# Optimization experiments

Hardware: AMD Instinct MI355X
Metric: run time of the kernel (lower is better)

## Reference

```python
import jax, jax.numpy as jnp
import numpy as np

D, U, NNZ, B = 8192, 4096, 1_700_000, 1024

def setup_inputs() -> dict:
    key = jax.random.key(0)
    k1, k2, k3, k4 = jax.random.split(key, 4)
    x = jax.random.normal(k1, (B, D), dtype=jnp.float32)
    kernel_vector = jax.random.normal(k2, (NNZ,), dtype=jnp.float32) * 0.02
    bias = jax.random.normal(k3, (U,), dtype=jnp.float32) * 0.01
    flat = jax.random.randint(k4, (NNZ,), 0, D * U)  # random sparsity pattern
    nonzero_ind = jnp.stack([flat // U, flat % U], axis=1).astype(jnp.int32)  # [NNZ, 2]
    return {"x": x, "kernel_vector": kernel_vector, "bias": bias, "nonzero_ind": nonzero_ind}

def reference(x, kernel_vector, bias, nonzero_ind):
    # scatter_nd: build dense (D, U) kernel from nonzero entries (duplicates add, as in tf.scatter_nd)
    W = jnp.zeros((D, U), dtype=kernel_vector.dtype).at[nonzero_ind[:, 0], nonzero_ind[:, 1]].add(kernel_vector)
    out = x @ W + bias  # [B, U]
    return jnp.tanh(out)
```

## Files before the change

### kernel.cpp

```cpp
#include <hip/hip_runtime.h>
#include <hip/hip_fp16.h>
#include <cmath>

#define DIM_M 1024
#define DIM_K 8192
#define DIM_N 4096
#define SPLIT 4
#define KSPL  (DIM_K / SPLIT)
#define BKT   64
#define NT    (KSPL / BKT)
#define NB    1024
#define EPB   8192

typedef __attribute__((ext_vector_type(8))) _Float16 half8;
typedef __attribute__((ext_vector_type(4))) float floatx4;

struct __align__(8) Half4 { __half2 a, b; };

__device__ inline void gload_lds16(const void* g, void* l) {
    __builtin_amdgcn_global_load_lds(
        (const __attribute__((address_space(1))) void*)g,
        (__attribute__((address_space(3))) void*)l, 16, 0, 0);
}

__global__ void cvt_f2h(const floatx4* __restrict__ in, Half4* __restrict__ out, int n4) {
    int i = blockIdx.x * blockDim.x + threadIdx.x;
    if (i < n4) {
        floatx4 f = in[i];
        Half4 h;
        h.a = __floats2half2_rn(f.x, f.y);
        h.b = __floats2half2_rn(f.z, f.w);
        out[i] = h;
    }
}

__global__ __launch_bounds__(512) void cluster_k(const int* __restrict__ ind,
                                                 const float* __restrict__ kv,
                                                 uint2* __restrict__ ebuf,
                                                 unsigned* __restrict__ ofs,
                                                 int nnz) {
    extern __shared__ char csm[];
    uint2*    buf = (uint2*)csm;
    unsigned* cur = (unsigned*)(csm + 65536);
    unsigned* ss  = (unsigned*)(csm + 69632);
    const int tid = threadIdx.x, blk = blockIdx.x;
    const int base = blk * EPB;
    const int lim = min(nnz - base, EPB);
    const int4*   ip = (const int4*)(ind + 2 * (size_t)base);
    const float2* vp = (const float2*)(kv + base);

    for (int i = tid; i < NB; i += 512) cur[i] = 0u;
    __syncthreads();
    for (int k2 = tid; k2 < lim / 2; k2 += 512) {
        int4 w = ip[k2];
        atomicAdd(&cur[w.y >> 2], 1u);
        atomicAdd(&cur[w.w >> 2], 1u);
    }
    if ((lim & 1) && tid == 0) {
        int u = ind[2 * (size_t)(base + lim - 1) + 1];
        atomicAdd(&cur[u >> 2], 1u);
    }
    __syncthreads();
    unsigned c0 = cur[2 * tid], c1 = cur[2 * tid + 1];
    unsigned own = c0 + c1;
    ss[tid] = own;
    __syncthreads();
    for (int off = 1; off < 512; off <<= 1) {
        unsigned t = (tid >= off) ? ss[tid - off] : 0u;
        __syncthreads();
        ss[tid] += t;
        __syncthreads();
    }
    unsigned e0 = ss[tid] - own;
    unsigned e1 = e0 + c0;
    __syncthreads();
    cur[2 * tid]     = e0;
    cur[2 * tid + 1] = e1;
    unsigned* obase = ofs + (size_t)blk * (NB + 1);
    obase[2 * tid]     = e0;
    obase[2 * tid + 1] = e1;
    if (tid == 511) obase[NB] = ss[511];
    __syncthreads();
    for (int k2 = tid; k2 < lim / 2; k2 += 512) {
        int4 w = ip[k2];
        float2 v = vp[k2];
        unsigned r0 = atomicAdd(&cur[w.y >> 2], 1u);
        buf[r0] = make_uint2(((unsigned)(w.y & 3) << 13) | (unsigned)w.x, __float_as_uint(v.x));
        unsigned r1 = atomicAdd(&cur[w.w >> 2], 1u);
        buf[r1] = make_uint2(((unsigned)(w.w & 3) << 13) | (unsigned)w.z, __float_as_uint(v.y));
    }
    if ((lim & 1) && tid == 0) {
        size_t e = (size_t)base + lim - 1;
        int d = ind[2 * e], u = ind[2 * e + 1];
        unsigned r = atomicAdd(&cur[u >> 2], 1u);
        buf[r] = make_uint2(((unsigned)(u & 3) << 13) | (unsigned)d, __float_as_uint(kv[e]));
    }
    __syncthreads();
    for (int j = tid; j < lim; j += 512)
        ebuf[(size_t)blk * EPB + j] = buf[j];
}

__global__ __launch_bounds__(512) void accum_k(const uint2* __restrict__ ebuf,
                                               const unsigned* __restrict__ ofs,
                                               int nblk,
                                               Half4* __restrict__ wh4) {
    extern __shared__ float reg[];
    floatx4* reg4 = (floatx4*)reg;
    const int tid = threadIdx.x, bin = blockIdx.x;
    for (int i = tid; i < 8192; i += 512) reg4[i] = floatx4{0.f, 0.f, 0.f, 0.f};
    __syncthreads();
    for (int sb = tid; sb < nblk; sb += 512) {
        const unsigned* ob = ofs + (size_t)sb * (NB + 1) + bin;
        unsigned o0 = ob[0], o1 = ob[1];
        const uint2* p = ebuf + (size_t)sb * EPB;
        for (unsigned e = o0; e < o1; ++e) {
            uint2 v = p[e];
            atomicAdd(&reg[v.x], __uint_as_float(v.y));
        }
    }
    __syncthreads();
    for (int i = tid; i < 8192; i += 512) {
        floatx4 f = reg4[i];
        Half4 h;
        h.a = __floats2half2_rn(f.x, f.y);
        h.b = __floats2half2_rn(f.z, f.w);
        wh4[(size_t)bin * 8192 + i] = h;
    }
}

__global__ __launch_bounds__(1024, 4) void gemm8_k(
    const _Float16* __restrict__ Ah,
    const _Float16* __restrict__ Bh,
    _Float16*       __restrict__ part)
{
    extern __shared__ char smem[];

    const int tid  = threadIdx.x;
    const int lane = tid & 63;
    const int wave = tid >> 6;

    const int bid = blockIdx.x;
    const int swz = (bid & 7) * 32 + (bid >> 3);
    const int n0  = (swz >> 4) * 256;
    const int rem = swz & 15;
    const int m0  = (rem >> 2) * 256;
    const int sp  = rem & 3;
    const size_t kbase = (size_t)sp * KSPL;

    const int srow = tid >> 3;
    const int sch  = (tid & 7) ^ (srow & 7);
    const _Float16* aSg = Ah + (size_t)(m0 + srow) * DIM_K + kbase + sch * 8;
    const _Float16* bSg = Bh + (size_t)(n0 + srow) * DIM_K + kbase + sch * 8;
    char* aLg = smem + wave * 1024;
    char* bLg = smem + 32768 + wave * 1024;

    const int wn  = wave & 3;
    const int wrm = wave >> 2;
    const int q   = lane >> 4;
    const int l7  = lane & 7;
    const char* aRd = smem + (wrm * 64 + (lane & 15)) * 128;
    const char* bRd = smem + 32768 + (wn * 64 + (lane & 15)) * 128;
    const int ch0 = ((0 * 4 + q) ^ l7) * 16;
    const int ch1 = ((1 * 4 + q) ^ l7) * 16;

    floatx4 acc[4][4] = {};
    half8 aF[4], bF[4];

#define STAGE(C)                                                              \
    { _Pragma("unroll") for (int p = 0; p < 2; ++p) {                         \
        gload_lds16(aSg + (size_t)p * (128 * DIM_K), aLg + (C) * 65536 + p * 16384); \
        gload_lds16(bSg + (size_t)p * (128 * DIM_K), bLg + (C) * 65536 + p * 16384); } \
      aSg += BKT; bSg += BKT; }

#define PH(C, CH)                                                             \
    { _Pragma("unroll") for (int i = 0; i < 4; ++i)                           \
        aF[i] = *(const half8*)(aRd + (C) * 65536 + i * 2048 + (CH));         \
      _Pragma("unroll") for (int i = 0; i < 4; ++i)                           \
        bF[i] = *(const half8*)(bRd + (C) * 65536 + i * 2048 + (CH));         \
      asm volatile("s_waitcnt lgkmcnt(0)" ::: "memory");                      \
      __builtin_amdgcn_sched_barrier(0);                                      \
      __builtin_amdgcn_s_setprio(1);                                          \
      _Pragma("unroll") for (int mi = 0; mi < 4; ++mi)                        \
        _Pragma("unroll") for (int ni = 0; ni < 4; ++ni)                      \
          acc[mi][ni] = __builtin_amdgcn_mfma_f32_16x16x32_f16(               \
              aF[mi], bF[ni], acc[mi][ni], 0, 0, 0);                          \
      __builtin_amdgcn_s_setprio(0); }

#define KTILE(C) PH(C, ch0) PH(C, ch1)

    STAGE(0)
    STAGE(1)
    asm volatile("s_waitcnt vmcnt(4)" ::: "memory");
    __builtin_amdgcn_s_barrier();

    for (int t2 = 0; t2 < NT / 2; ++t2) {
        KTILE(0)
        __builtin_amdgcn_s_barrier();
        if (t2 < NT / 2 - 1) {
            STAGE(0)
            asm volatile("s_waitcnt vmcnt(4)" ::: "memory");
        } else {
            asm volatile("s_waitcnt vmcnt(0)" ::: "memory");
        }
        __builtin_amdgcn_s_barrier();
        KTILE(1)
        if (t2 < NT / 2 - 1) {
            __builtin_amdgcn_s_barrier();
            STAGE(1)
            asm volatile("s_waitcnt vmcnt(4)" ::: "memory");
            __builtin_amdgcn_s_barrier();
        }
    }

#undef KTILE
#undef PH
#undef STAGE

    _Float16* pbase = part + (size_t)sp * DIM_M * DIM_N;
    #pragma unroll
    for (int ni = 0; ni < 4; ++ni) {
        const int col = n0 + wn * 64 + ni * 16 + (lane & 15);
        #pragma unroll
        for (int mi = 0; mi < 4; ++mi) {
            const int row = m0 + wrm * 64 + mi * 16 + (q << 2);
            #pragma unroll
            for (int r = 0; r < 4; ++r)
                pbase[(size_t)(row + r) * DIM_N + col] = (_Float16)acc[mi][ni][r];
        }
    }
}

__global__ void reduce_tanh(const Half4* __restrict__ part, const float* __restrict__ bias,
                            floatx4* __restrict__ out) {
    const int n4 = DIM_M * DIM_N / 4;
    int i = blockIdx.x * blockDim.x + threadIdx.x;
    if (i < n4) {
        float sx = 0.f, sy = 0.f, sz = 0.f, sw = 0.f;
        #pragma unroll
        for (int sp = 0; sp < SPLIT; ++sp) {
            Half4 p = part[(size_t)sp * n4 + i];
            float2 lo = __half22float2(p.a);
            float2 hi = __half22float2(p.b);
            sx += lo.x; sy += lo.y; sz += hi.x; sw += hi.y;
        }
        floatx4 b = ((const floatx4*)bias)[i & (DIM_N / 4 - 1)];
        floatx4 o;
        o.x = tanhf(sx + b.x);
        o.y = tanhf(sy + b.y);
        o.z = tanhf(sz + b.z);
        o.w = tanhf(sw + b.w);
        out[i] = o;
    }
}

extern "C" void kernel_launch(void* const* d_in, const int* in_sizes, int n_in,
                              void* d_out, int out_size, void* d_ws, size_t ws_size,
                              hipStream_t stream) {
    const float* x    = (const float*)d_in[0];
    const float* kv   = (const float*)d_in[1];
    const float* bias = (const float*)d_in[2];
    const int*   ind  = (const int*)d_in[3];
    float* out = (float*)d_out;
    const int nnz = in_sizes[1];

    char* ws = (char*)d_ws;
    _Float16* wh = (_Float16*)ws;
    const size_t whBytes = (size_t)DIM_N * DIM_K * 2;
    _Float16* xh = (_Float16*)(ws + whBytes);
    const size_t xhBytes = (size_t)DIM_M * DIM_K * 2;
    _Float16* part = (_Float16*)(ws + whBytes + xhBytes);
    const size_t partBytes = (size_t)SPLIT * DIM_M * DIM_N * 2;
    uint2* ebuf = (uint2*)(ws + whBytes + xhBytes + partBytes);
    const size_t ebufBytes = (size_t)16 << 20;
    unsigned* ofs = (unsigned*)(ws + whBytes + xhBytes + partBytes + ebufBytes);

    const int xN4 = (int)((size_t)DIM_M * DIM_K / 4);
    const int oN4 = DIM_M * DIM_N / 4;
    const int nblk = (nnz + EPB - 1) / EPB;

    cvt_f2h<<<(xN4 + 255) / 256, 256, 0, stream>>>((const floatx4*)x, (Half4*)xh, xN4);

    hipFuncSetAttribute((const void*)cluster_k,
                        hipFuncAttributeMaxDynamicSharedMemorySize, 71680);
    cluster_k<<<nblk, 512, 71680, stream>>>(ind, kv, ebuf, ofs, nnz);

    hipFuncSetAttribute((const void*)accum_k,
                        hipFuncAttributeMaxDynamicSharedMemorySize, 131072);
    accum_k<<<NB, 512, 131072, stream>>>(ebuf, ofs, nblk, (Half4*)wh);

    hipFuncSetAttribute((const void*)gemm8_k,
                        hipFuncAttributeMaxDynamicSharedMemorySize, 131072);
    gemm8_k<<<dim3(256), 1024, 131072, stream>>>(xh, wh, part);

    reduce_tanh<<<(oN4 + 255) / 256, 256, 0, stream>>>((const Half4*)part, bias, (floatx4*)out);
}
```

Baseline: 125.2 us.

## Fuse x fp16 conversion into cluster kernel and split accum work per bin

The separate fp32-to-fp16 conversion kernel for x is folded into cluster_k as extra blocks appended after the clustering blocks, so both jobs run in one launch and can overlap. Separately, accum_k now gives each source block's bin segment to two threads that take alternating entries, doubling the parallelism in the scatter-accumulate loop. The conversion blocks still request 70KB of LDS they do not use, which can limit how many blocks fit per CU. The accum change adds more LDS atomic contention.

```diff
diff --git a/kernel.cpp b/kernel.cpp
--- a/kernel.cpp
+++ b/kernel.cpp
@@ -11,6 +11,7 @@
 #define NT    (KSPL / BKT)
 #define NB    1024
 #define EPB   8192
+#define CVTB  1024
 
 typedef __attribute__((ext_vector_type(8))) _Float16 half8;
 typedef __attribute__((ext_vector_type(4))) float floatx4;
@@ -23,27 +24,35 @@
         (__attribute__((address_space(3))) void*)l, 16, 0, 0);
 }
 
-__global__ void cvt_f2h(const floatx4* __restrict__ in, Half4* __restrict__ out, int n4) {
-    int i = blockIdx.x * blockDim.x + threadIdx.x;
-    if (i < n4) {
-        floatx4 f = in[i];
-        Half4 h;
-        h.a = __floats2half2_rn(f.x, f.y);
-        h.b = __floats2half2_rn(f.z, f.w);
-        out[i] = h;
-    }
-}
-
 __global__ __launch_bounds__(512) void cluster_k(const int* __restrict__ ind,
                                                  const float* __restrict__ kv,
                                                  uint2* __restrict__ ebuf,
                                                  unsigned* __restrict__ ofs,
-                                                 int nnz) {
+                                                 int nnz, int nblk,
+                                                 const floatx4* __restrict__ xin,
+                                                 Half4* __restrict__ xout) {
     extern __shared__ char csm[];
+    const int tid = threadIdx.x;
+
+    if (blockIdx.x >= nblk) {
+        const int cb = blockIdx.x - nblk;
+        const int base = cb * 2048;
+        #pragma unroll
+        for (int j = 0; j < 4; ++j) {
+            int i = base + j * 512 + tid;
+            floatx4 f = xin[i];
+            Half4 h;
+            h.a = __floats2half2_rn(f.x, f.y);
+            h.b = __floats2half2_rn(f.z, f.w);
+            xout[i] = h;
+        }
+        return;
+    }
+
     uint2*    buf = (uint2*)csm;
     unsigned* cur = (unsigned*)(csm + 65536);
     unsigned* ss  = (unsigned*)(csm + 69632);
-    const int tid = threadIdx.x, blk = blockIdx.x;
+    const int blk = blockIdx.x;
     const int base = blk * EPB;
     const int lim = min(nnz - base, EPB);
     const int4*   ip = (const int4*)(ind + 2 * (size_t)base);
@@ -109,11 +118,12 @@
     const int tid = threadIdx.x, bin = blockIdx.x;
     for (int i = tid; i < 8192; i += 512) reg4[i] = floatx4{0.f, 0.f, 0.f, 0.f};
     __syncthreads();
-    for (int sb = tid; sb < nblk; sb += 512) {
+    for (int s2 = tid; s2 < 2 * nblk; s2 += 512) {
+        const int sb = s2 >> 1;
         const unsigned* ob = ofs + (size_t)sb * (NB + 1) + bin;
-        unsigned o0 = ob[0], o1 = ob[1];
+        unsigned o0 = ob[0] + (s2 & 1), o1 = ob[1];
         const uint2* p = ebuf + (size_t)sb * EPB;
-        for (unsigned e = o0; e < o1; ++e) {
+        for (unsigned e = o0; e < o1; e += 2) {
             uint2 v = p[e];
             atomicAdd(&reg[v.x], __uint_as_float(v.y));
         }
@@ -274,15 +284,13 @@
     const size_t ebufBytes = (size_t)16 << 20;
     unsigned* ofs = (unsigned*)(ws + whBytes + xhBytes + partBytes + ebufBytes);
 
-    const int xN4 = (int)((size_t)DIM_M * DIM_K / 4);
     const int oN4 = DIM_M * DIM_N / 4;
     const int nblk = (nnz + EPB - 1) / EPB;
 
-    cvt_f2h<<<(xN4 + 255) / 256, 256, 0, stream>>>((const floatx4*)x, (Half4*)xh, xN4);
-
     hipFuncSetAttribute((const void*)cluster_k,
                         hipFuncAttributeMaxDynamicSharedMemorySize, 71680);
-    cluster_k<<<nblk, 512, 71680, stream>>>(ind, kv, ebuf, ofs, nnz);
+    cluster_k<<<nblk + CVTB, 512, 71680, stream>>>(ind, kv, ebuf, ofs, nnz, nblk,
+                                                   (const floatx4*)x, (Half4*)xh);
 
     hipFuncSetAttribute((const void*)accum_k,
                         hipFuncAttributeMaxDynamicSharedMemorySize, 131072);
```

Result: faster. 115.9 us, median of 2 (-7.5%).
